# Performance work log

Measured on AMD Instinct MI355X. Metric: run time of the kernel, lower is better.

## Reference

```python
import jax, jax.numpy as jnp
import numpy as np
from jax import lax

T, B, D, H = 1024, 64, 512, 1024


def setup_inputs() -> dict:
    key = jax.random.key(0)
    ks = jax.random.split(key, 5)
    x = jax.random.normal(ks[0], (T, B, D), dtype=jnp.float32)
    W_ih_0 = jax.random.normal(ks[1], (H, D), dtype=jnp.float32) * (1.0 / np.sqrt(D))
    w_hh_0 = jax.random.uniform(ks[2], (H,), dtype=jnp.float32)
    b_0 = jnp.zeros((H,), dtype=jnp.float32)
    W_ih_1 = jax.random.normal(ks[3], (H, H), dtype=jnp.float32) * (1.0 / np.sqrt(H))
    w_hh_1 = jax.random.uniform(ks[4], (H,), dtype=jnp.float32)
    b_1 = jnp.zeros((H,), dtype=jnp.float32)
    return {"x": x, "W_ih_0": W_ih_0, "w_hh_0": w_hh_0, "b_0": b_0,
            "W_ih_1": W_ih_1, "w_hh_1": w_hh_1, "b_1": b_1}


def _indrnn_layer(x, W_ih, w_hh, b):
    # Hoist the input projection into one batched GEMM over all timesteps.
    pre = jnp.einsum('tbd,hd->tbh', x, W_ih) + b  # [T,B,H]
    h0 = jnp.zeros((x.shape[1], W_ih.shape[0]), dtype=x.dtype)

    def step(h, p):
        h_new = jnp.tanh(p + h * w_hh)  # diagonal recurrence
        return h_new, h_new

    _, out = lax.scan(step, h0, pre)  # out: [T,B,H]
    return out


def reference(x, W_ih_0, w_hh_0, b_0, W_ih_1, w_hh_1, b_1):
    out0 = _indrnn_layer(x, W_ih_0, w_hh_0, b_0)
    out1 = _indrnn_layer(out0, W_ih_1, w_hh_1, b_1)
    # Original returns (last-layer outputs, initial hidden) -- hidden is
    # the unchanged zeros tensor of shape [num_layers, B, H].
    hidden = jnp.zeros((2, x.shape[1], W_ih_0.shape[0]), dtype=x.dtype)
    return out1, hidden
```

## Files before the change

### kernel.cpp

```cpp
#include <hip/hip_runtime.h>
#include <hip/hip_fp16.h>
#include <cstdint>
#include <cstddef>

#define TT 1024
#define BB 64
#define DD 512
#define HH 1024
#define MM (TT * BB)

typedef _Float16 f16;
typedef _Float16 f16x8 __attribute__((ext_vector_type(8)));
typedef float f32x4 __attribute__((ext_vector_type(4)));

__global__ void cvt_f32_to_f16(const float* __restrict__ src,
                               f16* __restrict__ dst, int n) {
    int i = blockIdx.x * blockDim.x + threadIdx.x;
    int idx = i * 8;
    if (idx + 8 <= n) {
        float4 a = *reinterpret_cast<const float4*>(src + idx);
        float4 b = *reinterpret_cast<const float4*>(src + idx + 4);
        f16x8 o;
        o[0] = (f16)a.x; o[1] = (f16)a.y; o[2] = (f16)a.z; o[3] = (f16)a.w;
        o[4] = (f16)b.x; o[5] = (f16)b.y; o[6] = (f16)b.z; o[7] = (f16)b.w;
        *reinterpret_cast<f16x8*>(dst + idx) = o;
    } else {
        for (int k = idx; k < n; ++k) dst[k] = (f16)src[k];
    }
}

__device__ __forceinline__ void gload16(const void* g, void* l) {
    __builtin_amdgcn_global_load_lds(
        (const __attribute__((address_space(1))) void*)g,
        (__attribute__((address_space(3))) void*)l, 16, 0, 0);
}

__device__ __forceinline__ void stage128x64(const f16* __restrict__ G,
                                            int rowbase, int K, int kt,
                                            f16* lbuf, int tid) {
    #pragma unroll
    for (int j = 0; j < 4; ++j) {
        int p   = (j * 256 + tid) * 16;
        int row = p >> 7;
        int lc  = (p & 127) ^ ((row & 7) << 4);
        gload16(G + (size_t)(rowbase + row) * K + kt * 64 + (lc >> 1),
                (char*)lbuf + p);
    }
}

__device__ __forceinline__ f16x8 ldfrag(const f16* buf, int r, int s,
                                        int kg) {
    int c = ((s * 4 + kg) ^ (r & 7)) << 4;
    return *reinterpret_cast<const f16x8*>((const char*)buf + r * 128 + c);
}

template <typename TC>
__global__ __launch_bounds__(256, 4) void gemm5(
    const f16* __restrict__ A, const f16* __restrict__ W,
    const float* __restrict__ bias, TC* __restrict__ C,
    int M, int N, int K) {
    __shared__ f16 lds[2][128 * 64];

    const int tid  = threadIdx.x;
    const int lane = tid & 63;
    const int wid  = tid >> 6;
    const int wm   = wid >> 1;
    const int wn   = wid & 1;
    const int lr   = lane & 15;
    const int kg   = lane >> 4;

    const int nwg = gridDim.x;
    int bid = blockIdx.x;
    int wg  = (nwg % 8 == 0) ? ((bid & 7) * (nwg >> 3) + (bid >> 3)) : bid;
    const int ncol = N >> 7;
    const int brow = (wg / ncol) << 7;
    const int bcol = (wg % ncol) << 7;

    const int NT = K >> 6;

    f32x4 acc[4][4] = {};

    for (int t = 0; t < NT; ++t) {
        __syncthreads();
        stage128x64(A, brow, K, t, lds[0], tid);
        stage128x64(W, bcol, K, t, lds[1], tid);
        __syncthreads();

        #pragma unroll
        for (int s = 0; s < 2; ++s) {
            f16x8 af[4], bf[4];
            #pragma unroll
            for (int m = 0; m < 4; ++m)
                af[m] = ldfrag(lds[0], wm * 64 + m * 16 + lr, s, kg);
            #pragma unroll
            for (int n = 0; n < 4; ++n)
                bf[n] = ldfrag(lds[1], wn * 64 + n * 16 + lr, s, kg);
            #pragma unroll
            for (int m = 0; m < 4; ++m)
                #pragma unroll
                for (int n = 0; n < 4; ++n)
                    acc[m][n] = __builtin_amdgcn_mfma_f32_16x16x32_f16(
                        af[m], bf[n], acc[m][n], 0, 0, 0);
        }
    }

    if constexpr (sizeof(TC) == 2) {
        f16* Ct = &lds[0][0];
        __syncthreads();
        #pragma unroll
        for (int fn = 0; fn < 4; ++fn) {
            int col = wn * 64 + fn * 16 + lr;
            float bv = bias[bcol + col];
            #pragma unroll
            for (int fm = 0; fm < 4; ++fm) {
                int row0 = wm * 64 + fm * 16 + kg * 4;
                #pragma unroll
                for (int j = 0; j < 4; ++j) {
                    int r  = row0 + j;
                    int pb = r * 256 + ((col * 2) ^ ((r & 7) << 4));
                    *(f16*)((char*)Ct + pb) = (f16)(acc[fm][fn][j] + bv);
                }
            }
        }
        __syncthreads();
        #pragma unroll
        for (int i = 0; i < 8; ++i) {
            int e   = (i * 256 + tid) * 16;
            int row = e >> 8;
            int cb  = e & 255;
            int pb  = row * 256 + (cb ^ ((row & 7) << 4));
            f16x8 v = *(const f16x8*)((const char*)Ct + pb);
            *reinterpret_cast<f16x8*>(
                (f16*)C + (size_t)(brow + row) * N + bcol + (cb >> 1)) = v;
        }
    } else {
        #pragma unroll
        for (int fn = 0; fn < 4; ++fn) {
            int col = bcol + wn * 64 + fn * 16 + lr;
            float bv = bias[col];
            #pragma unroll
            for (int fm = 0; fm < 4; ++fm) {
                int row0 = brow + wm * 64 + fm * 16 + kg * 4;
                #pragma unroll
                for (int j = 0; j < 4; ++j)
                    C[(size_t)(row0 + j) * N + col] = (TC)(acc[fm][fn][j] + bv);
            }
        }
    }
}

__device__ __forceinline__ float fast_tanh(float x) {
    float e = __builtin_amdgcn_exp2f(x * 2.8853900817779268f);
    float r = __builtin_amdgcn_rcpf(e + 1.0f);
    return 1.0f - 2.0f * r;
}

template <typename TI, typename TO, int PF>
__global__ __launch_bounds__(256) void scan_kernel(
    const TI* __restrict__ pre, const float* __restrict__ w,
    TO* __restrict__ out) {
    const int S = BB * HH;
    const int idx = blockIdx.x * blockDim.x + threadIdx.x;
    const float wv = w[idx & (HH - 1)];
    const TI* p = pre + idx;
    TO* o = out + idx;

    float buf[PF];
    #pragma unroll
    for (int i = 0; i < PF; ++i) buf[i] = (float)p[(size_t)i * S];

    float h = 0.f;
    for (int t0 = 0; t0 < TT; t0 += PF) {
        float nbuf[PF];
        #pragma unroll
        for (int i = 0; i < PF; ++i) {
            int tp = t0 + PF + i;
            tp = (tp < TT - 1) ? tp : (TT - 1);
            nbuf[i] = (float)p[(size_t)tp * S];
        }
        #pragma unroll
        for (int i = 0; i < PF; ++i) {
            h = fast_tanh(fmaf(h, wv, buf[i]));
            o[(size_t)(t0 + i) * S] = (TO)h;
        }
        #pragma unroll
        for (int i = 0; i < PF; ++i) buf[i] = nbuf[i];
    }
}

__global__ void zero_kernel(float* p, int n) {
    int i = blockIdx.x * blockDim.x + threadIdx.x;
    if (i < n) p[i] = 0.f;
}

extern "C" void kernel_launch(void* const* d_in, const int* in_sizes, int n_in,
                              void* d_out, int out_size, void* d_ws, size_t ws_size,
                              hipStream_t stream) {
    const float* x  = (const float*)d_in[0];
    const float* W0 = (const float*)d_in[1];
    const float* w0 = (const float*)d_in[2];
    const float* b0 = (const float*)d_in[3];
    const float* W1 = (const float*)d_in[4];
    const float* w1 = (const float*)d_in[5];
    const float* b1 = (const float*)d_in[6];
    float* out = (float*)d_out;

    const size_t SZ_big = (size_t)MM * HH * sizeof(f16);
    const size_t O_W0   = SZ_big;
    const size_t O_W1   = O_W0 + (size_t)HH * DD * sizeof(f16);
    const size_t O_pre1 = O_W1 + (size_t)HH * HH * sizeof(f16);
    const bool f16pre1  = (ws_size >= O_pre1 + SZ_big);

    f16* big   = (f16*)d_ws;
    f16* W0h   = (f16*)((char*)d_ws + O_W0);
    f16* W1h   = (f16*)((char*)d_ws + O_W1);
    f16* pre1h = (f16*)((char*)d_ws + O_pre1);

    const int nwg = (MM / 128) * (HH / 128);

    cvt_f32_to_f16<<<(MM * DD) / 8 / 256, 256, 0, stream>>>(x, big, MM * DD);
    cvt_f32_to_f16<<<(HH * DD) / 8 / 256, 256, 0, stream>>>(W0, W0h, HH * DD);
    cvt_f32_to_f16<<<(HH * HH) / 8 / 256, 256, 0, stream>>>(W1, W1h, HH * HH);

    gemm5<f16><<<nwg, 256, 0, stream>>>(big, W0h, b0, (f16*)d_out, MM, HH, DD);

    scan_kernel<f16, f16, 32><<<(BB * HH) / 256, 256, 0, stream>>>(
        (const f16*)d_out, w0, big);

    if (f16pre1) {
        gemm5<f16><<<nwg, 256, 0, stream>>>(big, W1h, b1, pre1h, MM, HH, HH);
        scan_kernel<f16, float, 32><<<(BB * HH) / 256, 256, 0, stream>>>(
            pre1h, w1, out);
    } else {
        gemm5<float><<<nwg, 256, 0, stream>>>(big, W1h, b1, out, MM, HH, HH);
        scan_kernel<float, float, 32><<<(BB * HH) / 256, 256, 0, stream>>>(
            out, w1, out);
    }

    zero_kernel<<<(2 * BB * HH) / 256, 256, 0, stream>>>(
        out + (size_t)MM * HH, 2 * BB * HH);
}
```

Measured before the change: 427.1 us.

## Fuse x f32-to-f16 conversion into GEMM staging, merge weight casts, fold zeroing

The first GEMM now loads fp32 x directly and converts it to fp16 while staging into LDS, which removes the separate conversion kernel and its 64M-element round trip through memory. The two weight conversions are merged into one launch, and zeroing the hidden tail is folded into the final scan kernel, so two more launches go away. In exchange, the first GEMM's A staging becomes synchronous register loads plus conversion instead of async global_load_lds, and it reads twice the bytes per tile, which can slow the GEMM's inner loop.

```diff
diff --git a/kernel.cpp b/kernel.cpp
--- a/kernel.cpp
+++ b/kernel.cpp
@@ -10,23 +10,26 @@
 #define MM (TT * BB)
 
 typedef _Float16 f16;
+typedef _Float16 f16x4 __attribute__((ext_vector_type(4)));
 typedef _Float16 f16x8 __attribute__((ext_vector_type(8)));
 typedef float f32x4 __attribute__((ext_vector_type(4)));
 
-__global__ void cvt_f32_to_f16(const float* __restrict__ src,
-                               f16* __restrict__ dst, int n) {
+__global__ void cvt_weights(const float* __restrict__ W0, f16* __restrict__ W0h,
+                            int n0, const float* __restrict__ W1,
+                            f16* __restrict__ W1h) {
     int i = blockIdx.x * blockDim.x + threadIdx.x;
     int idx = i * 8;
-    if (idx + 8 <= n) {
-        float4 a = *reinterpret_cast<const float4*>(src + idx);
-        float4 b = *reinterpret_cast<const float4*>(src + idx + 4);
-        f16x8 o;
-        o[0] = (f16)a.x; o[1] = (f16)a.y; o[2] = (f16)a.z; o[3] = (f16)a.w;
-        o[4] = (f16)b.x; o[5] = (f16)b.y; o[6] = (f16)b.z; o[7] = (f16)b.w;
-        *reinterpret_cast<f16x8*>(dst + idx) = o;
-    } else {
-        for (int k = idx; k < n; ++k) dst[k] = (f16)src[k];
-    }
+    const float* s;
+    f16* d;
+    int off;
+    if (idx < n0) { s = W0; d = W0h; off = idx; }
+    else          { s = W1; d = W1h; off = idx - n0; }
+    float4 a = *reinterpret_cast<const float4*>(s + off);
+    float4 b = *reinterpret_cast<const float4*>(s + off + 4);
+    f16x8 o;
+    o[0] = (f16)a.x; o[1] = (f16)a.y; o[2] = (f16)a.z; o[3] = (f16)a.w;
+    o[4] = (f16)b.x; o[5] = (f16)b.y; o[6] = (f16)b.z; o[7] = (f16)b.w;
+    *reinterpret_cast<f16x8*>(d + off) = o;
 }
 
 __device__ __forceinline__ void gload16(const void* g, void* l) {
@@ -35,9 +38,9 @@
         (__attribute__((address_space(3))) void*)l, 16, 0, 0);
 }
 
-__device__ __forceinline__ void stage128x64(const f16* __restrict__ G,
-                                            int rowbase, int K, int kt,
-                                            f16* lbuf, int tid) {
+__device__ __forceinline__ void stage_tile(const f16* __restrict__ G,
+                                           int rowbase, int K, int kt,
+                                           f16* lbuf, int tid) {
     #pragma unroll
     for (int j = 0; j < 4; ++j) {
         int p   = (j * 256 + tid) * 16;
@@ -48,15 +51,31 @@
     }
 }
 
+__device__ __forceinline__ void stage_tile(const float* __restrict__ G,
+                                           int rowbase, int K, int kt,
+                                           f16* lbuf, int tid) {
+    #pragma unroll
+    for (int j = 0; j < 8; ++j) {
+        int p   = (j * 256 + tid) * 8;
+        int row = p >> 7;
+        int lc  = (p & 127) ^ ((row & 7) << 4);
+        float4 v = *reinterpret_cast<const float4*>(
+            G + (size_t)(rowbase + row) * K + kt * 64 + (lc >> 1));
+        f16x4 h;
+        h[0] = (f16)v.x; h[1] = (f16)v.y; h[2] = (f16)v.z; h[3] = (f16)v.w;
+        *reinterpret_cast<f16x4*>((char*)lbuf + p) = h;
+    }
+}
+
 __device__ __forceinline__ f16x8 ldfrag(const f16* buf, int r, int s,
                                         int kg) {
     int c = ((s * 4 + kg) ^ (r & 7)) << 4;
     return *reinterpret_cast<const f16x8*>((const char*)buf + r * 128 + c);
 }
 
-template <typename TC>
-__global__ __launch_bounds__(256, 4) void gemm5(
-    const f16* __restrict__ A, const f16* __restrict__ W,
+template <typename TA, typename TC>
+__global__ __launch_bounds__(256, 4) void gemm6(
+    const TA* __restrict__ A, const f16* __restrict__ W,
     const float* __restrict__ bias, TC* __restrict__ C,
     int M, int N, int K) {
     __shared__ f16 lds[2][128 * 64];
@@ -82,8 +101,8 @@
 
     for (int t = 0; t < NT; ++t) {
         __syncthreads();
-        stage128x64(A, brow, K, t, lds[0], tid);
-        stage128x64(W, bcol, K, t, lds[1], tid);
+        stage_tile(A, brow, K, t, lds[0], tid);
+        stage_tile(W, bcol, K, t, lds[1], tid);
         __syncthreads();
 
         #pragma unroll
@@ -155,7 +174,7 @@
     return 1.0f - 2.0f * r;
 }
 
-template <typename TI, typename TO, int PF>
+template <typename TI, typename TO, int PF, bool ZTAIL>
 __global__ __launch_bounds__(256) void scan_kernel(
     const TI* __restrict__ pre, const float* __restrict__ w,
     TO* __restrict__ out) {
@@ -185,6 +204,10 @@
         }
         #pragma unroll
         for (int i = 0; i < PF; ++i) buf[i] = nbuf[i];
+    }
+    if constexpr (ZTAIL) {
+        o[(size_t)TT * S] = (TO)0.f;
+        o[(size_t)(TT + 1) * S] = (TO)0.f;
     }
 }
 
@@ -211,32 +234,31 @@
     const size_t O_pre1 = O_W1 + (size_t)HH * HH * sizeof(f16);
     const bool f16pre1  = (ws_size >= O_pre1 + SZ_big);
 
-    f16* big   = (f16*)d_ws;
+    f16* out0  = (f16*)d_ws;
     f16* W0h   = (f16*)((char*)d_ws + O_W0);
     f16* W1h   = (f16*)((char*)d_ws + O_W1);
     f16* pre1h = (f16*)((char*)d_ws + O_pre1);
 
     const int nwg = (MM / 128) * (HH / 128);
 
-    cvt_f32_to_f16<<<(MM * DD) / 8 / 256, 256, 0, stream>>>(x, big, MM * DD);
-    cvt_f32_to_f16<<<(HH * DD) / 8 / 256, 256, 0, stream>>>(W0, W0h, HH * DD);
-    cvt_f32_to_f16<<<(HH * HH) / 8 / 256, 256, 0, stream>>>(W1, W1h, HH * HH);
-
-    gemm5<f16><<<nwg, 256, 0, stream>>>(big, W0h, b0, (f16*)d_out, MM, HH, DD);
-
-    scan_kernel<f16, f16, 32><<<(BB * HH) / 256, 256, 0, stream>>>(
-        (const f16*)d_out, w0, big);
+    cvt_weights<<<(HH * DD + HH * HH) / 8 / 256, 256, 0, stream>>>(
+        W0, W0h, HH * DD, W1, W1h);
+
+    gemm6<float, f16><<<nwg, 256, 0, stream>>>(
+        x, W0h, b0, (f16*)d_out, MM, HH, DD);
+
+    scan_kernel<f16, f16, 32, false><<<(BB * HH) / 256, 256, 0, stream>>>(
+        (const f16*)d_out, w0, out0);
 
     if (f16pre1) {
-        gemm5<f16><<<nwg, 256, 0, stream>>>(big, W1h, b1, pre1h, MM, HH, HH);
-        scan_kernel<f16, float, 32><<<(BB * HH) / 256, 256, 0, stream>>>(
+        gemm6<f16, f16><<<nwg, 256, 0, stream>>>(
+            out0, W1h, b1, pre1h, MM, HH, HH);
+        scan_kernel<f16, float, 32, true><<<(BB * HH) / 256, 256, 0, stream>>>(
             pre1h, w1, out);
     } else {
-        gemm5<float><<<nwg, 256, 0, stream>>>(big, W1h, b1, out, MM, HH, HH);
-        scan_kernel<float, float, 32><<<(BB * HH) / 256, 256, 0, stream>>>(
+        gemm6<f16, float><<<nwg, 256, 0, stream>>>(
+            out0, W1h, b1, out, MM, HH, HH);
+        scan_kernel<float, float, 32, true><<<(BB * HH) / 256, 256, 0, stream>>>(
             out, w1, out);
     }
-
-    zero_kernel<<<(2 * BB * HH) / 256, 256, 0, stream>>>(
-        out + (size_t)MM * HH, 2 * BB * HH);
-}
+}
```

New measurement: 508.8 us. +19.1%, slower.
